# Optimization experiments

Measured on AMD Instinct MI355X. Metric: run time of the kernel, lower is better.

## Reference

```python
import jax, jax.numpy as jnp
import numpy as np

N_NODES = 100000
N_EDGES = 6400000


def setup_inputs() -> dict:
    key = jax.random.key(0)
    k = jax.random.split(key, 5)
    x = jax.random.normal(k[0], (N_NODES, 4), dtype=jnp.float32)
    edge_index = jax.random.randint(k[1], (2, N_EDGES), 0, N_NODES, dtype=jnp.int32)
    # Glorot-style init for GCN linear weights
    W1 = jax.random.normal(k[2], (4, 16), dtype=jnp.float32) * (1.0 / np.sqrt(4.0))
    b1 = jnp.zeros((16,), dtype=jnp.float32)
    W2 = jax.random.normal(k[3], (16, 2), dtype=jnp.float32) * (1.0 / np.sqrt(16.0))
    b2 = jnp.zeros((2,), dtype=jnp.float32)
    return {"x": x, "edge_index": edge_index, "W1": W1, "b1": b1, "W2": W2, "b2": b2}


def _gcn_conv(x, src, dst, deg_inv_sqrt, W, b):
    """One GCNConv layer: linear transform -> symmetric-normalized scatter-add -> bias.

    src, dst already include self-loops; deg_inv_sqrt precomputed on the
    self-loop-augmented graph (matches PyG GCNConv defaults).
    """
    n = x.shape[0]
    h = x @ W                                   # [N, F_out]
    coef = deg_inv_sqrt[src] * deg_inv_sqrt[dst]  # [E+N]
    msg = h[src] * coef[:, None]                # gather + scale, [E+N, F_out]
    out = jax.ops.segment_sum(msg, dst, num_segments=n)  # scatter-add
    return out + b


def reference(x, edge_index, W1, b1, W2, b2):
    n = x.shape[0]
    loop = jnp.arange(n, dtype=edge_index.dtype)
    src = jnp.concatenate([edge_index[0], loop])  # add self-loops
    dst = jnp.concatenate([edge_index[1], loop])
    deg = jax.ops.segment_sum(jnp.ones_like(dst, dtype=x.dtype), dst, num_segments=n)
    deg_inv_sqrt = jnp.where(deg > 0, jax.lax.rsqrt(deg), 0.0)

    h = jax.nn.relu(_gcn_conv(x, src, dst, deg_inv_sqrt, W1, b1))
    return _gcn_conv(h, src, dst, deg_inv_sqrt, W2, b2)
```

## Files before the change

kernel.cpp:

```cpp
#include <hip/hip_runtime.h>

#define TPB 256
#define CSH 10
#define CN 1024
#define NBC_MAX 128
#define STILE 8192
#define EPT (STILE / TPB)

#define P2 8
#define SB_SH 8
#define SBN_MAX 512
#define CAP 28

#define B20 1048576
#define S1F 131072.0f
#define S2F 8192.0f

typedef unsigned long long u64;

__device__ __forceinline__ unsigned enc_fx(float v, float scale) {
    int xi = __float2int_rn(v * scale);
    xi = max(-(B20 - 1), min(B20 - 1, xi));
    return (unsigned)(xi + B20);
}

__global__ void k_zero(int* __restrict__ p, int n) {
    int i = blockIdx.x * blockDim.x + threadIdx.x;
    if (i < n) p[i] = 0;
}

__global__ void k_passCk(const int* __restrict__ src, const int* __restrict__ dst,
                         unsigned* __restrict__ packed, int* __restrict__ chunklT,
                         int* __restrict__ chunkpT, int E, int NBC, int ntiles) {
    __shared__ unsigned stage[STILE];
    __shared__ int cnt[NBC_MAX], lb[NBC_MAX];
    int tb = blockIdx.x * STILE;
    int te = min(E, tb + STILE);
    if (threadIdx.x < NBC_MAX) cnt[threadIdx.x] = 0;
    __syncthreads();
    unsigned pk[EPT];
    int br[EPT];
#pragma unroll
    for (int u = 0; u < EPT; u++) {
        int i = tb + u * TPB + (int)threadIdx.x;
        br[u] = -1;
        if (i < te) {
            int d = dst[i];
            int b = d >> CSH;
            pk[u] = ((unsigned)src[i] << CSH) | (unsigned)(d & (CN - 1));
            int r = atomicAdd(&cnt[b], 1);
            br[u] = b | (r << 7);
        }
    }
    __syncthreads();
    if (threadIdx.x < (unsigned)NBC) {
        int b = threadIdx.x;
        int sum = 0;
        for (int j = 0; j < b; j++) sum += cnt[j];
        lb[b] = sum;
        chunklT[(size_t)b * ntiles + blockIdx.x] = cnt[b];
        chunkpT[(size_t)b * ntiles + blockIdx.x] = tb + sum;
    }
    __syncthreads();
#pragma unroll
    for (int u = 0; u < EPT; u++) {
        if (br[u] >= 0) {
            int b = br[u] & (NBC_MAX - 1);
            stage[lb[b] + (br[u] >> 7)] = pk[u];
        }
    }
    __syncthreads();
    for (int i = threadIdx.x; i < te - tb; i += TPB)
        packed[tb + i] = stage[i];
}

__global__ void k_p2a(const unsigned* __restrict__ packed, const int* __restrict__ chunklT,
                      const int* __restrict__ chunkpT, int* __restrict__ h,
                      int* __restrict__ deg, int ntiles, int SBN, int N) {
    __shared__ int hist[SBN_MAX];
    __shared__ int dcnt[CN];
    int b = blockIdx.x / P2, p = blockIdx.x - b * P2;
    for (int i = threadIdx.x; i < SBN_MAX; i += TPB) hist[i] = 0;
    for (int i = threadIdx.x; i < CN; i += TPB) dcnt[i] = 0;
    __syncthreads();
    int t0 = (int)((long long)ntiles * p / P2);
    int t1 = (int)((long long)ntiles * (p + 1) / P2);
    int wv = threadIdx.x >> 6, lane = threadIdx.x & 63;
    const int* cl = chunklT + (size_t)b * ntiles;
    const int* cp = chunkpT + (size_t)b * ntiles;
    for (int t = t0 + wv; t < t1; t += 4) {
        int len = cl[t];
        if (!len) continue;
        int pos = cp[t];
        for (int i = lane; i < len; i += 64) {
            unsigned pk = packed[pos + i];
            atomicAdd(&hist[pk >> (CSH + SB_SH)], 1);
            atomicAdd(&dcnt[pk & (CN - 1)], 1);
        }
    }
    __syncthreads();
    int* hp = h + (size_t)blockIdx.x * SBN;
    for (int i = threadIdx.x; i < SBN; i += TPB) hp[i] = hist[i];
    int node0 = b << CSH;
    for (int i = threadIdx.x; i < CN; i += TPB)
        if (dcnt[i] && node0 + i < N) atomicAdd(&deg[node0 + i], dcnt[i]);
}

__global__ void k_scan1(const int* __restrict__ h, int* __restrict__ bsize, int SBN) {
    __shared__ int red[TPB];
    int b = blockIdx.x;
    const int* hb = h + (size_t)b * P2 * SBN;
    int n = P2 * SBN;
    int sum = 0;
    for (int i = threadIdx.x; i < n; i += TPB) sum += hb[i];
    red[threadIdx.x] = sum;
    __syncthreads();
    for (int off = TPB / 2; off > 0; off >>= 1) {
        if (threadIdx.x < off) red[threadIdx.x] += red[threadIdx.x + off];
        __syncthreads();
    }
    if (threadIdx.x == 0) bsize[b] = red[0];
}

__global__ void k_scanbase(const int* __restrict__ bsize, int* __restrict__ base, int NBC) {
    __shared__ int s[NBC_MAX];
    int t = threadIdx.x;
    if (t < NBC_MAX) s[t] = (t < NBC) ? bsize[t] : 0;
    __syncthreads();
    for (int off = 1; off < NBC_MAX; off <<= 1) {
        int v = 0;
        if (t < NBC_MAX && t >= off) v = s[t - off];
        __syncthreads();
        if (t < NBC_MAX) s[t] += v;
        __syncthreads();
    }
    if (t < NBC) base[t] = (t == 0) ? 0 : s[t - 1];
    if (t == 0) base[NBC] = s[NBC - 1];
}

__global__ void k_scan3(int* __restrict__ h, const int* __restrict__ base, int SBN) {
    __shared__ int tsum[TPB];
    int b = blockIdx.x;
    int* hb = h + (size_t)b * P2 * SBN;
    int n = SBN * P2;
    int per = (n + TPB - 1) / TPB;
    int i0 = threadIdx.x * per;
    int vals[16];
    int sum = 0;
    for (int k = 0; k < per; k++) {
        int idx = i0 + k;
        int v = 0;
        if (idx < n) {
            int sb = idx >> 3, p = idx & (P2 - 1);
            v = hb[p * SBN + sb];
        }
        vals[k] = v;
        sum += v;
    }
    tsum[threadIdx.x] = sum;
    __syncthreads();
    for (int off = 1; off < TPB; off <<= 1) {
        int v = (threadIdx.x >= off) ? tsum[threadIdx.x - off] : 0;
        __syncthreads();
        tsum[threadIdx.x] += v;
        __syncthreads();
    }
    int run = base[b] + ((threadIdx.x == 0) ? 0 : tsum[threadIdx.x - 1]);
    for (int k = 0; k < per; k++) {
        int idx = i0 + k;
        if (idx < n) {
            int sb = idx >> 3, p = idx & (P2 - 1);
            hb[p * SBN + sb] = run;
            run += vals[k];
        }
    }
}

__global__ void k_p2b(const unsigned* __restrict__ packed, const int* __restrict__ chunklT,
                      const int* __restrict__ chunkpT, const int* __restrict__ off,
                      unsigned* __restrict__ packed2, int ntiles, int SBN) {
    __shared__ unsigned binbuf[SBN_MAX * CAP];
    __shared__ int cnt[SBN_MAX];
    __shared__ int goff[SBN_MAX];
    int b = blockIdx.x / P2, p = blockIdx.x - b * P2;
    const int* offp = off + (size_t)blockIdx.x * SBN;
    for (int i = threadIdx.x; i < SBN_MAX; i += TPB) {
        cnt[i] = 0;
        goff[i] = (i < SBN) ? offp[i] : 0;
    }
    __syncthreads();
    int t0 = (int)((long long)ntiles * p / P2);
    int t1 = (int)((long long)ntiles * (p + 1) / P2);
    int wv = threadIdx.x >> 6, lane = threadIdx.x & 63;
    const int* cl = chunklT + (size_t)b * ntiles;
    const int* cp = chunkpT + (size_t)b * ntiles;
    for (int t = t0 + wv; t < t1; t += 4) {
        int len = cl[t];
        if (!len) continue;
        int pos = cp[t];
        for (int i = lane; i < len; i += 64) {
            unsigned pk = packed[pos + i];
            int sb = pk >> (CSH + SB_SH);
            int r = atomicAdd(&cnt[sb], 1);
            if (r < CAP) binbuf[sb * CAP + r] = pk;
            else packed2[goff[sb] + r] = pk;
        }
    }
    __syncthreads();
    for (int sb = wv; sb < SBN; sb += 4) {
        int c = min(cnt[sb], CAP);
        int gb = goff[sb];
        for (int i = lane; i < c; i += 64)
            packed2[gb + i] = binbuf[sb * CAP + i];
    }
}

__global__ void k_prepv(const float* __restrict__ x, const int* __restrict__ deg,
                        float* __restrict__ xs, unsigned* __restrict__ xse, int N) {
    int v = blockIdx.x * blockDim.x + threadIdx.x;
    if (v >= N) return;
    float di = rsqrtf((float)(deg[v] + 1));
    float4 xv = ((const float4*)x)[v];
    xv.x *= di; xv.y *= di; xv.z *= di; xv.w *= di;
    ((float4*)xs)[v] = xv;
    uint4 e;
    e.x = enc_fx(xv.x, S1F); e.y = enc_fx(xv.y, S1F);
    e.z = enc_fx(xv.z, S1F); e.w = enc_fx(xv.w, S1F);
    ((uint4*)xse)[v] = e;
}

#define AGG1_AT(pkv, gv) { int n_ = (int)((pkv) & (CN - 1)) * 3; \
    atomicAdd(&acc[n_],     (u64)(gv).x | ((u64)(gv).y << 32)); \
    atomicAdd(&acc[n_ + 1], (u64)(gv).z | ((u64)(gv).w << 32)); }

__global__ void k_agg1n(const unsigned* __restrict__ packed2, const int* __restrict__ base,
                        const unsigned* __restrict__ xse, u64* __restrict__ partial1, int S1) {
    __shared__ u64 acc[CN * 3];
    for (int i = threadIdx.x; i < CN * 3; i += TPB) acc[i] = 0ULL;
    __syncthreads();
    int b = blockIdx.x / S1, s = blockIdx.x - b * S1;
    int lo = base[b], sz = base[b + 1] - lo;
    int i0 = lo + (int)((long long)sz * s / S1);
    int i1 = lo + (int)((long long)sz * (s + 1) / S1);
    const uint4* xse4 = (const uint4*)xse;
    int i = i0 + (int)threadIdx.x;
    for (; i + 3 * TPB < i1; i += 4 * TPB) {
        unsigned pa = packed2[i];
        unsigned pb = packed2[i + TPB];
        unsigned pc = packed2[i + 2 * TPB];
        unsigned pd = packed2[i + 3 * TPB];
        uint4 ga = xse4[pa >> CSH];
        uint4 gb = xse4[pb >> CSH];
        uint4 gc = xse4[pc >> CSH];
        uint4 gd = xse4[pd >> CSH];
        AGG1_AT(pa, ga); AGG1_AT(pb, gb); AGG1_AT(pc, gc); AGG1_AT(pd, gd);
    }
    for (; i < i1; i += TPB) {
        unsigned pk = packed2[i];
        uint4 g = xse4[pk >> CSH];
        AGG1_AT(pk, g);
    }
    __syncthreads();
    u64* p = partial1 + (size_t)blockIdx.x * (CN * 2);
    for (int i2 = threadIdx.x; i2 < CN * 2; i2 += TPB)
        p[i2] = acc[(i2 >> 1) * 3 + (i2 & 1)];
}

__global__ void k_comb1q(const u64* __restrict__ partial1,
                         const float* __restrict__ xs, const int* __restrict__ deg,
                         const float* __restrict__ W1, const float* __restrict__ b1,
                         const float* __restrict__ W2,
                         float* __restrict__ hs2f, unsigned* __restrict__ hs2e,
                         int S1, int N) {
    __shared__ float w1[64], w2[32], bb[16];
    if (threadIdx.x < 64) w1[threadIdx.x] = W1[threadIdx.x];
    if (threadIdx.x < 32) w2[threadIdx.x] = W2[threadIdx.x];
    if (threadIdx.x < 16) bb[threadIdx.x] = b1[threadIdx.x];
    __syncthreads();
    int v = blockIdx.x * blockDim.x + threadIdx.x;
    if (v >= N) return;
    int b = v >> CSH, lv = v & (CN - 1);
    u64 a01 = 0, a23 = 0;
    for (int s = 0; s < S1; s++) {
        const u64* q = partial1 + ((size_t)(b * S1 + s) * CN + lv) * 2;
        a01 += q[0];
        a23 += q[1];
    }
    int dg = deg[v];
    long long bias = (long long)dg << 20;
    const float inv = 1.0f / S1F;
    float f0 = (float)((long long)(a01 & 0xffffffffULL) - bias) * inv;
    float f1 = (float)((long long)(a01 >> 32) - bias) * inv;
    float f2 = (float)((long long)(a23 & 0xffffffffULL) - bias) * inv;
    float f3 = (float)((long long)(a23 >> 32) - bias) * inv;
    float4 self = ((const float4*)xs)[v];
    float di = rsqrtf((float)(dg + 1));
    float v0 = (f0 + self.x) * di, v1 = (f1 + self.y) * di;
    float v2 = (f2 + self.z) * di, v3 = (f3 + self.w) * di;
    float s0 = 0.f, s1 = 0.f;
#pragma unroll
    for (int j = 0; j < 16; j++) {
        float h = v0 * w1[j] + v1 * w1[16 + j] + v2 * w1[32 + j] + v3 * w1[48 + j] + bb[j];
        h = fmaxf(h, 0.0f);
        s0 += h * w2[2 * j];
        s1 += h * w2[2 * j + 1];
    }
    s0 *= di; s1 *= di;
    ((float2*)hs2f)[v] = make_float2(s0, s1);
    uint2 e;
    e.x = enc_fx(s0, S2F);
    e.y = enc_fx(s1, S2F);
    ((uint2*)hs2e)[v] = e;
}

__global__ void k_agg2n(const unsigned* __restrict__ packed2, const int* __restrict__ base,
                        const unsigned* __restrict__ hs2e, u64* __restrict__ partial2, int S2) {
    __shared__ u64 acc[CN];
    for (int i = threadIdx.x; i < CN; i += TPB) acc[i] = 0ULL;
    __syncthreads();
    int b = blockIdx.x / S2, s = blockIdx.x - b * S2;
    int lo = base[b], sz = base[b + 1] - lo;
    int i0 = lo + (int)((long long)sz * s / S2);
    int i1 = lo + (int)((long long)sz * (s + 1) / S2);
    const uint2* h2 = (const uint2*)hs2e;
    int i = i0 + (int)threadIdx.x;
    for (; i + 3 * TPB < i1; i += 4 * TPB) {
        unsigned pa = packed2[i];
        unsigned pb = packed2[i + TPB];
        unsigned pc = packed2[i + 2 * TPB];
        unsigned pd = packed2[i + 3 * TPB];
        uint2 ga = h2[pa >> CSH];
        uint2 gb = h2[pb >> CSH];
        uint2 gc = h2[pc >> CSH];
        uint2 gd = h2[pd >> CSH];
        atomicAdd(&acc[pa & (CN - 1)], (u64)ga.x | ((u64)ga.y << 32));
        atomicAdd(&acc[pb & (CN - 1)], (u64)gb.x | ((u64)gb.y << 32));
        atomicAdd(&acc[pc & (CN - 1)], (u64)gc.x | ((u64)gc.y << 32));
        atomicAdd(&acc[pd & (CN - 1)], (u64)gd.x | ((u64)gd.y << 32));
    }
    for (; i < i1; i += TPB) {
        unsigned pk = packed2[i];
        uint2 g = h2[pk >> CSH];
        atomicAdd(&acc[pk & (CN - 1)], (u64)g.x | ((u64)g.y << 32));
    }
    __syncthreads();
    u64* p = partial2 + (size_t)blockIdx.x * CN;
    for (int i2 = threadIdx.x; i2 < CN; i2 += TPB) p[i2] = acc[i2];
}

__global__ void k_comb2q(const u64* __restrict__ partial2,
                         const float* __restrict__ hs2f, const int* __restrict__ deg,
                         const float* __restrict__ b2, float* __restrict__ out,
                         int S2, int N) {
    int v = blockIdx.x * blockDim.x + threadIdx.x;
    if (v >= N) return;
    int b = v >> CSH, lv = v & (CN - 1);
    u64 t = 0;
    for (int s = 0; s < S2; s++)
        t += partial2[(size_t)(b * S2 + s) * CN + lv];
    int dg = deg[v];
    long long bias = (long long)dg << 20;
    const float inv = 1.0f / S2F;
    float f0 = (float)((long long)(t & 0xffffffffULL) - bias) * inv;
    float f1 = (float)((long long)(t >> 32) - bias) * inv;
    float2 self = ((const float2*)hs2f)[v];
    float di = rsqrtf((float)(dg + 1));
    ((float2*)out)[v] = make_float2((f0 + self.x) * di + b2[0],
                                    (f1 + self.y) * di + b2[1]);
}


__global__ void k_deg_fb(const int* __restrict__ dst, int* __restrict__ deg, int E) {
    int i = blockIdx.x * blockDim.x + threadIdx.x;
    if (i < E) atomicAdd(&deg[dst[i]], 1);
}
__global__ void k_dis_fb(const int* __restrict__ deg, float* __restrict__ dis, int N) {
    int v = blockIdx.x * blockDim.x + threadIdx.x;
    if (v < N) dis[v] = rsqrtf((float)(deg[v] + 1));
}
__global__ void k_lin1_fb(const float* __restrict__ x, const float* __restrict__ W1,
                          const float* __restrict__ dis, float* __restrict__ hs1,
                          float* __restrict__ agg1, int N) {
    __shared__ float w[64];
    if (threadIdx.x < 64) w[threadIdx.x] = W1[threadIdx.x];
    __syncthreads();
    int v = blockIdx.x * blockDim.x + threadIdx.x;
    if (v >= N) return;
    float4 xv = ((const float4*)x)[v];
    float d = dis[v];
#pragma unroll
    for (int j = 0; j < 16; j++) {
        float h = (xv.x * w[j] + xv.y * w[16 + j] + xv.z * w[32 + j] + xv.w * w[48 + j]) * d;
        hs1[v * 16 + j] = h;
        agg1[v * 16 + j] = h;
    }
}
__global__ void k_scat1_fb(const int* __restrict__ src, const int* __restrict__ dst,
                           const float* __restrict__ hs1, float* __restrict__ agg1, int E4) {
    int t = blockIdx.x * blockDim.x + threadIdx.x;
    if (t >= E4) return;
    int e = t >> 2, q = t & 3;
    int s = src[e], d = dst[e];
    float4 m = ((const float4*)hs1)[s * 4 + q];
    float* a = agg1 + (size_t)d * 16 + q * 4;
    atomicAdd(a + 0, m.x); atomicAdd(a + 1, m.y);
    atomicAdd(a + 2, m.z); atomicAdd(a + 3, m.w);
}
__global__ void k_lin2_fb(const float* __restrict__ agg1, const float* __restrict__ dis,
                          const float* __restrict__ b1, const float* __restrict__ W2,
                          float* __restrict__ hs2, float* __restrict__ agg2, int N) {
    __shared__ float w[32];
    __shared__ float bb[16];
    if (threadIdx.x < 32) w[threadIdx.x] = W2[threadIdx.x];
    if (threadIdx.x < 16) bb[threadIdx.x] = b1[threadIdx.x];
    __syncthreads();
    int v = blockIdx.x * blockDim.x + threadIdx.x;
    if (v >= N) return;
    float d = dis[v];
    float a0 = 0.f, a1 = 0.f;
#pragma unroll
    for (int k = 0; k < 16; k++) {
        float r = fmaxf(agg1[v * 16 + k] * d + bb[k], 0.0f);
        a0 += r * w[k * 2 + 0];
        a1 += r * w[k * 2 + 1];
    }
    float2 hv = make_float2(a0 * d, a1 * d);
    ((float2*)hs2)[v] = hv;
    ((float2*)agg2)[v] = hv;
}
__global__ void k_scat2_fb(const int* __restrict__ src, const int* __restrict__ dst,
                           const float* __restrict__ hs2, float* __restrict__ agg2, int E) {
    int e = blockIdx.x * blockDim.x + threadIdx.x;
    if (e >= E) return;
    int s = src[e], d = dst[e];
    float2 m = ((const float2*)hs2)[s];
    atomicAdd(&agg2[d * 2 + 0], m.x);
    atomicAdd(&agg2[d * 2 + 1], m.y);
}
__global__ void k_out_fb(const float* __restrict__ agg2, const float* __restrict__ dis,
                         const float* __restrict__ b2, float* __restrict__ out, int N) {
    int v = blockIdx.x * blockDim.x + threadIdx.x;
    if (v >= N) return;
    float d = dis[v];
    out[v * 2 + 0] = agg2[v * 2 + 0] * d + b2[0];
    out[v * 2 + 1] = agg2[v * 2 + 1] * d + b2[1];
}


extern "C" void kernel_launch(void* const* d_in, const int* in_sizes, int n_in,
                              void* d_out, int out_size, void* d_ws, size_t ws_size,
                              hipStream_t stream) {
    const float* x  = (const float*)d_in[0];
    const int*   ei = (const int*)d_in[1];
    const float* W1 = (const float*)d_in[2];
    const float* b1 = (const float*)d_in[3];
    const float* W2 = (const float*)d_in[4];
    const float* b2 = (const float*)d_in[5];

    const int N = in_sizes[0] / 4;
    const int E = in_sizes[1] / 2;
    const int* src = ei;
    const int* dst = ei + E;
    float* outp = (float*)d_out;

    auto align = [](size_t v) { return (v + 255) & ~(size_t)255; };
    const int NBC = (N + CN - 1) >> CSH;
    const int SBN = (N + 255) >> SB_SH;
    const int gN  = (N + TPB - 1) / TPB;
    const int ntiles = (E + STILE - 1) / STILE;
    const bool src_fits = (size_t)N <= ((size_t)1 << (32 - CSH));
    const bool fx_safe = (long long)E <= (long long)N * 512;

    const int S1 = 16, S2 = 16;
    size_t part1_bytes = (size_t)NBC * S1 * CN * 16;
    size_t part2_bytes = (size_t)NBC * S2 * CN * 8;
    size_t pkA_bytes = (size_t)E * 4;
    if (part1_bytes > pkA_bytes) pkA_bytes = part1_bytes;
    if (part2_bytes > pkA_bytes) pkA_bytes = part2_bytes;

    size_t need_new = align(pkA_bytes)
                    + align((size_t)E * 4)
                    + align((size_t)N * 16)
                    + align((size_t)N * 16)
                    + align((size_t)N * 8)
                    + align((size_t)N * 8)
                    + align((size_t)N * 4)
                    + align((size_t)ntiles * NBC * 4)
                    + align((size_t)ntiles * NBC * 4)
                    + align((size_t)NBC * P2 * SBN * 4)
                    + align((size_t)NBC * 4)
                    + align((size_t)(NBC + 1) * 4);

    if (ws_size >= need_new && NBC <= NBC_MAX && SBN <= SBN_MAX && src_fits && fx_safe) {
        char* ws = (char*)d_ws;
        unsigned* packed = (unsigned*)ws;
        u64* partial1 = (u64*)ws;
        u64* partial2 = (u64*)ws;
        ws += align(pkA_bytes);
        unsigned* packed2 = (unsigned*)ws; ws += align((size_t)E * 4);
        float* xs    = (float*)ws;    ws += align((size_t)N * 16);
        unsigned* xse = (unsigned*)ws; ws += align((size_t)N * 16);
        float* hs2f  = (float*)ws;    ws += align((size_t)N * 8);
        unsigned* hs2e = (unsigned*)ws; ws += align((size_t)N * 8);
        int* deg     = (int*)ws;      ws += align((size_t)N * 4);
        int* chunklT = (int*)ws;      ws += align((size_t)ntiles * NBC * 4);
        int* chunkpT = (int*)ws;      ws += align((size_t)ntiles * NBC * 4);
        int* h       = (int*)ws;      ws += align((size_t)NBC * P2 * SBN * 4);
        int* bsize   = (int*)ws;      ws += align((size_t)NBC * 4);
        int* base    = (int*)ws;      ws += align((size_t)(NBC + 1) * 4);

        k_zero<<<gN, TPB, 0, stream>>>(deg, N);
        k_passCk<<<ntiles, TPB, 0, stream>>>(src, dst, packed, chunklT, chunkpT, E, NBC, ntiles);
        k_p2a<<<NBC * P2, TPB, 0, stream>>>(packed, chunklT, chunkpT, h, deg, ntiles, SBN, N);
        k_scan1<<<NBC, TPB, 0, stream>>>(h, bsize, SBN);
        k_scanbase<<<1, TPB, 0, stream>>>(bsize, base, NBC);
        k_scan3<<<NBC, TPB, 0, stream>>>(h, base, SBN);
        k_p2b<<<NBC * P2, TPB, 0, stream>>>(packed, chunklT, chunkpT, h, packed2, ntiles, SBN);
        k_prepv<<<gN, TPB, 0, stream>>>(x, deg, xs, xse, N);
        k_agg1n<<<NBC * S1, TPB, 0, stream>>>(packed2, base, xse, partial1, S1);
        k_comb1q<<<gN, TPB, 0, stream>>>(partial1, xs, deg, W1, b1, W2, hs2f, hs2e, S1, N);
        k_agg2n<<<NBC * S2, TPB, 0, stream>>>(packed2, base, hs2e, partial2, S2);
        k_comb2q<<<gN, TPB, 0, stream>>>(partial2, hs2f, deg, b2, outp, S2, N);
    } else {
        char* ws = (char*)d_ws;
        int*   deg  = (int*)ws;   ws += align((size_t)N * 4);
        float* dis  = (float*)ws; ws += align((size_t)N * 4);
        float* hs1  = (float*)ws; ws += align((size_t)N * 16 * 4);
        float* agg1 = (float*)ws; ws += align((size_t)N * 16 * 4);
        float* hs2  = (float*)ws; ws += align((size_t)N * 2 * 4);
        float* agg2 = (float*)ws; ws += align((size_t)N * 2 * 4);
        int gE = (E + TPB - 1) / TPB;
        int gE4 = ((size_t)E * 4 + TPB - 1) / TPB;

        k_zero<<<gN, TPB, 0, stream>>>(deg, N);
        k_deg_fb<<<gE, TPB, 0, stream>>>(dst, deg, E);
        k_dis_fb<<<gN, TPB, 0, stream>>>(deg, dis, N);
        k_lin1_fb<<<gN, TPB, 0, stream>>>(x, W1, dis, hs1, agg1, N);
        k_scat1_fb<<<gE4, TPB, 0, stream>>>(src, dst, hs1, agg1, E * 4);
        k_lin2_fb<<<gN, TPB, 0, stream>>>(agg1, dis, b1, W2, hs2, agg2, N);
        k_scat2_fb<<<gE, TPB, 0, stream>>>(src, dst, hs2, agg2, E);
        k_out_fb<<<gN, TPB, 0, stream>>>(agg2, dis, b2, outp, N);
    }
}
```

Baseline: 273.6 us.

## Replace tile-chunk bucketing with global histogram and contiguous per-bucket scatter

The first sort pass now runs a global coarse histogram over dst, scans it, and scatters edges into contiguous per-bucket regions using atomic reservations. The per-tile chunk length and position tables are removed, along with the per-chunk iteration in the second-pass kernels. Those kernels can now stream over a contiguous range with 4-way unrolled loads, and the scan1 kernel goes away. This costs an extra full read of dst for the histogram and global atomics on bucket cursors, and the order of edges within a bucket is no longer deterministic.

```diff
diff --git a/kernel.cpp b/kernel.cpp
--- a/kernel.cpp
+++ b/kernel.cpp
@@ -10,7 +10,6 @@
 #define P2 8
 #define SB_SH 8
 #define SBN_MAX 512
-#define CAP 28
 
 #define B20 1048576
 #define S1F 131072.0f
@@ -29,11 +28,51 @@
     if (i < n) p[i] = 0;
 }
 
-__global__ void k_passCk(const int* __restrict__ src, const int* __restrict__ dst,
-                         unsigned* __restrict__ packed, int* __restrict__ chunklT,
-                         int* __restrict__ chunkpT, int E, int NBC, int ntiles) {
+__global__ void k_zero2(int* __restrict__ a, int na, int* __restrict__ b, int nb) {
+    int i = blockIdx.x * blockDim.x + threadIdx.x;
+    if (i < na) a[i] = 0;
+    if (i < nb) b[i] = 0;
+}
+
+__global__ void k_hist0(const int* __restrict__ dst, int* __restrict__ hist0,
+                        int NBC, int E) {
+    __shared__ int hh[NBC_MAX];
+    for (int i = threadIdx.x; i < NBC_MAX; i += TPB) hh[i] = 0;
+    __syncthreads();
+    int stride = gridDim.x * blockDim.x;
+    for (int i = blockIdx.x * blockDim.x + threadIdx.x; i < E; i += stride)
+        atomicAdd(&hh[dst[i] >> CSH], 1);
+    __syncthreads();
+    for (int i = threadIdx.x; i < NBC; i += TPB)
+        if (hh[i]) atomicAdd(&hist0[i], hh[i]);
+}
+
+__global__ void k_scanbase(const int* __restrict__ bsize, int* __restrict__ base,
+                           int* __restrict__ cur, int NBC) {
+    __shared__ int s[NBC_MAX];
+    int t = threadIdx.x;
+    if (t < NBC_MAX) s[t] = (t < NBC) ? bsize[t] : 0;
+    __syncthreads();
+    for (int off = 1; off < NBC_MAX; off <<= 1) {
+        int v = 0;
+        if (t < NBC_MAX && t >= off) v = s[t - off];
+        __syncthreads();
+        if (t < NBC_MAX) s[t] += v;
+        __syncthreads();
+    }
+    if (t < NBC) {
+        int b = (t == 0) ? 0 : s[t - 1];
+        base[t] = b;
+        cur[t] = b;
+    }
+    if (t == 0) base[NBC] = s[NBC - 1];
+}
+
+__global__ void k_bscat(const int* __restrict__ src, const int* __restrict__ dst,
+                        int* __restrict__ cur, unsigned* __restrict__ packed,
+                        int E, int NBC) {
     __shared__ unsigned stage[STILE];
-    __shared__ int cnt[NBC_MAX], lb[NBC_MAX];
+    __shared__ int cnt[NBC_MAX], lb[NBC_MAX], resv[NBC_MAX];
     int tb = blockIdx.x * STILE;
     int te = min(E, tb + STILE);
     if (threadIdx.x < NBC_MAX) cnt[threadIdx.x] = 0;
@@ -58,8 +97,7 @@
         int sum = 0;
         for (int j = 0; j < b; j++) sum += cnt[j];
         lb[b] = sum;
-        chunklT[(size_t)b * ntiles + blockIdx.x] = cnt[b];
-        chunkpT[(size_t)b * ntiles + blockIdx.x] = tb + sum;
+        resv[b] = cnt[b] ? atomicAdd(&cur[b], cnt[b]) : 0;
     }
     __syncthreads();
 #pragma unroll
@@ -70,72 +108,49 @@
         }
     }
     __syncthreads();
-    for (int i = threadIdx.x; i < te - tb; i += TPB)
-        packed[tb + i] = stage[i];
-}
-
-__global__ void k_p2a(const unsigned* __restrict__ packed, const int* __restrict__ chunklT,
-                      const int* __restrict__ chunkpT, int* __restrict__ h,
-                      int* __restrict__ deg, int ntiles, int SBN, int N) {
-    __shared__ int hist[SBN_MAX];
+    int wv = threadIdx.x >> 6, lane = threadIdx.x & 63;
+    for (int b = wv; b < NBC; b += 4) {
+        int c = cnt[b];
+        if (!c) continue;
+        int gb = resv[b], s0 = lb[b];
+        for (int i = lane; i < c; i += 64)
+            packed[gb + i] = stage[s0 + i];
+    }
+}
+
+__global__ void k_p2hist(const unsigned* __restrict__ packed, const int* __restrict__ base,
+                         int* __restrict__ h, int* __restrict__ deg, int SBN, int N) {
+    __shared__ int hsb[SBN_MAX];
     __shared__ int dcnt[CN];
     int b = blockIdx.x / P2, p = blockIdx.x - b * P2;
-    for (int i = threadIdx.x; i < SBN_MAX; i += TPB) hist[i] = 0;
+    for (int i = threadIdx.x; i < SBN_MAX; i += TPB) hsb[i] = 0;
     for (int i = threadIdx.x; i < CN; i += TPB) dcnt[i] = 0;
     __syncthreads();
-    int t0 = (int)((long long)ntiles * p / P2);
-    int t1 = (int)((long long)ntiles * (p + 1) / P2);
-    int wv = threadIdx.x >> 6, lane = threadIdx.x & 63;
-    const int* cl = chunklT + (size_t)b * ntiles;
-    const int* cp = chunkpT + (size_t)b * ntiles;
-    for (int t = t0 + wv; t < t1; t += 4) {
-        int len = cl[t];
-        if (!len) continue;
-        int pos = cp[t];
-        for (int i = lane; i < len; i += 64) {
-            unsigned pk = packed[pos + i];
-            atomicAdd(&hist[pk >> (CSH + SB_SH)], 1);
-            atomicAdd(&dcnt[pk & (CN - 1)], 1);
-        }
+    int lo = base[b], sz = base[b + 1] - lo;
+    int i0 = lo + (int)((long long)sz * p / P2);
+    int i1 = lo + (int)((long long)sz * (p + 1) / P2);
+    int i = i0 + (int)threadIdx.x;
+    for (; i + 3 * TPB < i1; i += 4 * TPB) {
+        unsigned pa = packed[i];
+        unsigned pb = packed[i + TPB];
+        unsigned pc = packed[i + 2 * TPB];
+        unsigned pd = packed[i + 3 * TPB];
+        atomicAdd(&hsb[pa >> (CSH + SB_SH)], 1); atomicAdd(&dcnt[pa & (CN - 1)], 1);
+        atomicAdd(&hsb[pb >> (CSH + SB_SH)], 1); atomicAdd(&dcnt[pb & (CN - 1)], 1);
+        atomicAdd(&hsb[pc >> (CSH + SB_SH)], 1); atomicAdd(&dcnt[pc & (CN - 1)], 1);
+        atomicAdd(&hsb[pd >> (CSH + SB_SH)], 1); atomicAdd(&dcnt[pd & (CN - 1)], 1);
+    }
+    for (; i < i1; i += TPB) {
+        unsigned pk = packed[i];
+        atomicAdd(&hsb[pk >> (CSH + SB_SH)], 1);
+        atomicAdd(&dcnt[pk & (CN - 1)], 1);
     }
     __syncthreads();
     int* hp = h + (size_t)blockIdx.x * SBN;
-    for (int i = threadIdx.x; i < SBN; i += TPB) hp[i] = hist[i];
+    for (int i2 = threadIdx.x; i2 < SBN; i2 += TPB) hp[i2] = hsb[i2];
     int node0 = b << CSH;
-    for (int i = threadIdx.x; i < CN; i += TPB)
-        if (dcnt[i] && node0 + i < N) atomicAdd(&deg[node0 + i], dcnt[i]);
-}
-
-__global__ void k_scan1(const int* __restrict__ h, int* __restrict__ bsize, int SBN) {
-    __shared__ int red[TPB];
-    int b = blockIdx.x;
-    const int* hb = h + (size_t)b * P2 * SBN;
-    int n = P2 * SBN;
-    int sum = 0;
-    for (int i = threadIdx.x; i < n; i += TPB) sum += hb[i];
-    red[threadIdx.x] = sum;
-    __syncthreads();
-    for (int off = TPB / 2; off > 0; off >>= 1) {
-        if (threadIdx.x < off) red[threadIdx.x] += red[threadIdx.x + off];
-        __syncthreads();
-    }
-    if (threadIdx.x == 0) bsize[b] = red[0];
-}
-
-__global__ void k_scanbase(const int* __restrict__ bsize, int* __restrict__ base, int NBC) {
-    __shared__ int s[NBC_MAX];
-    int t = threadIdx.x;
-    if (t < NBC_MAX) s[t] = (t < NBC) ? bsize[t] : 0;
-    __syncthreads();
-    for (int off = 1; off < NBC_MAX; off <<= 1) {
-        int v = 0;
-        if (t < NBC_MAX && t >= off) v = s[t - off];
-        __syncthreads();
-        if (t < NBC_MAX) s[t] += v;
-        __syncthreads();
-    }
-    if (t < NBC) base[t] = (t == 0) ? 0 : s[t - 1];
-    if (t == 0) base[NBC] = s[NBC - 1];
+    for (int i2 = threadIdx.x; i2 < CN; i2 += TPB)
+        if (dcnt[i2] && node0 + i2 < N) atomicAdd(&deg[node0 + i2], dcnt[i2]);
 }
 
 __global__ void k_scan3(int* __restrict__ h, const int* __restrict__ base, int SBN) {
@@ -176,42 +191,43 @@
     }
 }
 
-__global__ void k_p2b(const unsigned* __restrict__ packed, const int* __restrict__ chunklT,
-                      const int* __restrict__ chunkpT, const int* __restrict__ off,
-                      unsigned* __restrict__ packed2, int ntiles, int SBN) {
-    __shared__ unsigned binbuf[SBN_MAX * CAP];
-    __shared__ int cnt[SBN_MAX];
+__global__ void k_p2scat(const unsigned* __restrict__ packed, const int* __restrict__ base,
+                         const int* __restrict__ h, unsigned* __restrict__ packed2,
+                         int SBN) {
     __shared__ int goff[SBN_MAX];
+    __shared__ int cnt2[SBN_MAX];
     int b = blockIdx.x / P2, p = blockIdx.x - b * P2;
-    const int* offp = off + (size_t)blockIdx.x * SBN;
+    const int* hp = h + (size_t)blockIdx.x * SBN;
     for (int i = threadIdx.x; i < SBN_MAX; i += TPB) {
-        cnt[i] = 0;
-        goff[i] = (i < SBN) ? offp[i] : 0;
-    }
-    __syncthreads();
-    int t0 = (int)((long long)ntiles * p / P2);
-    int t1 = (int)((long long)ntiles * (p + 1) / P2);
-    int wv = threadIdx.x >> 6, lane = threadIdx.x & 63;
-    const int* cl = chunklT + (size_t)b * ntiles;
-    const int* cp = chunkpT + (size_t)b * ntiles;
-    for (int t = t0 + wv; t < t1; t += 4) {
-        int len = cl[t];
-        if (!len) continue;
-        int pos = cp[t];
-        for (int i = lane; i < len; i += 64) {
-            unsigned pk = packed[pos + i];
-            int sb = pk >> (CSH + SB_SH);
-            int r = atomicAdd(&cnt[sb], 1);
-            if (r < CAP) binbuf[sb * CAP + r] = pk;
-            else packed2[goff[sb] + r] = pk;
-        }
-    }
-    __syncthreads();
-    for (int sb = wv; sb < SBN; sb += 4) {
-        int c = min(cnt[sb], CAP);
-        int gb = goff[sb];
-        for (int i = lane; i < c; i += 64)
-            packed2[gb + i] = binbuf[sb * CAP + i];
+        cnt2[i] = 0;
+        goff[i] = (i < SBN) ? hp[i] : 0;
+    }
+    __syncthreads();
+    int lo = base[b], sz = base[b + 1] - lo;
+    int i0 = lo + (int)((long long)sz * p / P2);
+    int i1 = lo + (int)((long long)sz * (p + 1) / P2);
+    int i = i0 + (int)threadIdx.x;
+    for (; i + 3 * TPB < i1; i += 4 * TPB) {
+        unsigned pa = packed[i];
+        unsigned pb = packed[i + TPB];
+        unsigned pc = packed[i + 2 * TPB];
+        unsigned pd = packed[i + 3 * TPB];
+        int sa = pa >> (CSH + SB_SH), sb_ = pb >> (CSH + SB_SH);
+        int sc = pc >> (CSH + SB_SH), sd = pd >> (CSH + SB_SH);
+        int ra = atomicAdd(&cnt2[sa], 1);
+        int rb = atomicAdd(&cnt2[sb_], 1);
+        int rc = atomicAdd(&cnt2[sc], 1);
+        int rd = atomicAdd(&cnt2[sd], 1);
+        packed2[goff[sa] + ra] = pa;
+        packed2[goff[sb_] + rb] = pb;
+        packed2[goff[sc] + rc] = pc;
+        packed2[goff[sd] + rd] = pd;
+    }
+    for (; i < i1; i += TPB) {
+        unsigned pk = packed[i];
+        int sb2 = pk >> (CSH + SB_SH);
+        int r = atomicAdd(&cnt2[sb2], 1);
+        packed2[goff[sb2] + r] = pk;
     }
 }
 
@@ -465,7 +481,8 @@
 
     auto align = [](size_t v) { return (v + 255) & ~(size_t)255; };
     const int NBC = (N + CN - 1) >> CSH;
-    const int SBN = (N + 255) >> SB_SH;
+    const int SBN = (N + (1 << SB_SH) - 1) >> SB_SH;
+    const int NC  = NBC * P2 * SBN;
     const int gN  = (N + TPB - 1) / TPB;
     const int ntiles = (E + STILE - 1) / STILE;
     const bool src_fits = (size_t)N <= ((size_t)1 << (32 - CSH));
@@ -485,9 +502,8 @@
                     + align((size_t)N * 8)
                     + align((size_t)N * 8)
                     + align((size_t)N * 4)
-                    + align((size_t)ntiles * NBC * 4)
-                    + align((size_t)ntiles * NBC * 4)
-                    + align((size_t)NBC * P2 * SBN * 4)
+                    + align((size_t)NC * 4)
+                    + align((size_t)NBC * 4)
                     + align((size_t)NBC * 4)
                     + align((size_t)(NBC + 1) * 4);
 
@@ -503,19 +519,18 @@
         float* hs2f  = (float*)ws;    ws += align((size_t)N * 8);
         unsigned* hs2e = (unsigned*)ws; ws += align((size_t)N * 8);
         int* deg     = (int*)ws;      ws += align((size_t)N * 4);
-        int* chunklT = (int*)ws;      ws += align((size_t)ntiles * NBC * 4);
-        int* chunkpT = (int*)ws;      ws += align((size_t)ntiles * NBC * 4);
-        int* h       = (int*)ws;      ws += align((size_t)NBC * P2 * SBN * 4);
-        int* bsize   = (int*)ws;      ws += align((size_t)NBC * 4);
+        int* h       = (int*)ws;      ws += align((size_t)NC * 4);
+        int* hist0   = (int*)ws;      ws += align((size_t)NBC * 4);
+        int* cur     = (int*)ws;      ws += align((size_t)NBC * 4);
         int* base    = (int*)ws;      ws += align((size_t)(NBC + 1) * 4);
 
-        k_zero<<<gN, TPB, 0, stream>>>(deg, N);
-        k_passCk<<<ntiles, TPB, 0, stream>>>(src, dst, packed, chunklT, chunkpT, E, NBC, ntiles);
-        k_p2a<<<NBC * P2, TPB, 0, stream>>>(packed, chunklT, chunkpT, h, deg, ntiles, SBN, N);
-        k_scan1<<<NBC, TPB, 0, stream>>>(h, bsize, SBN);
-        k_scanbase<<<1, TPB, 0, stream>>>(bsize, base, NBC);
+        k_zero2<<<gN, TPB, 0, stream>>>(deg, N, hist0, NBC);
+        k_hist0<<<1024, TPB, 0, stream>>>(dst, hist0, NBC, E);
+        k_scanbase<<<1, TPB, 0, stream>>>(hist0, base, cur, NBC);
+        k_bscat<<<ntiles, TPB, 0, stream>>>(src, dst, cur, packed, E, NBC);
+        k_p2hist<<<NBC * P2, TPB, 0, stream>>>(packed, base, h, deg, SBN, N);
         k_scan3<<<NBC, TPB, 0, stream>>>(h, base, SBN);
-        k_p2b<<<NBC * P2, TPB, 0, stream>>>(packed, chunklT, chunkpT, h, packed2, ntiles, SBN);
+        k_p2scat<<<NBC * P2, TPB, 0, stream>>>(packed, base, h, packed2, SBN);
         k_prepv<<<gN, TPB, 0, stream>>>(x, deg, xs, xse, N);
         k_agg1n<<<NBC * S1, TPB, 0, stream>>>(packed2, base, xse, partial1, S1);
         k_comb1q<<<gN, TPB, 0, stream>>>(partial1, xs, deg, W1, b1, W2, hs2f, hs2e, S1, N);
```

New measurement: 265.9 us. 2.8% less time.
